# Performance work log

Measured on AMD Instinct MI355X. Metric: run time of the kernel, lower is better.

Reference implementation:

```python
import jax, jax.numpy as jnp
import numpy as np

HIDDEN = 1024
VOCAB = 50257


def setup_inputs() -> dict:
    key = jax.random.key(0)
    ks = jax.random.split(key, 9)
    s = 0.02
    return {
        "token": jax.random.randint(ks[0], (1,), 0, VOCAB, dtype=jnp.int64),
        "hidden": jax.random.normal(ks[1], (1, 1, HIDDEN), dtype=jnp.float32),
        "emb": jax.random.normal(ks[2], (VOCAB, HIDDEN), dtype=jnp.float32) * s,
        "w_ih": jax.random.normal(ks[3], (3 * HIDDEN, HIDDEN), dtype=jnp.float32) * s,
        "w_hh": jax.random.normal(ks[4], (3 * HIDDEN, HIDDEN), dtype=jnp.float32) * s,
        "b_ih": jax.random.normal(ks[5], (3 * HIDDEN,), dtype=jnp.float32) * s,
        "b_hh": jax.random.normal(ks[6], (3 * HIDDEN,), dtype=jnp.float32) * s,
        "w_out": jax.random.normal(ks[7], (VOCAB, HIDDEN), dtype=jnp.float32) * s,
        "b_out": jax.random.normal(ks[8], (VOCAB,), dtype=jnp.float32) * s,
    }


def reference(token, hidden, emb, w_ih, w_hh, b_ih, b_hh, w_out, b_out):
    # embed + relu: [1, H]
    x = jax.nn.relu(emb[token].reshape(1, HIDDEN))
    h = hidden[0]  # [1, H]
    # single-step GRU (PyTorch gate order r, z, n; separate biases)
    gi = x @ w_ih.T + b_ih  # [1, 3H]
    gh = h @ w_hh.T + b_hh  # [1, 3H]
    i_r, i_z, i_n = jnp.split(gi, 3, axis=-1)
    h_r, h_z, h_n = jnp.split(gh, 3, axis=-1)
    r = jax.nn.sigmoid(i_r + h_r)
    z = jax.nn.sigmoid(i_z + h_z)
    n = jnp.tanh(i_n + r * h_n)
    h_new = (1.0 - z) * n + z * h  # [1, H]
    # output projection + log-softmax over vocab
    logits = h_new @ w_out.T + b_out  # [1, V]
    logp = jax.nn.log_softmax(logits, axis=1)
    return logp, h_new[None]  # ([1, V], [1, 1, H])
```

## Files before the change

kernel.cpp:

```cpp
#include <hip/hip_runtime.h>
#include <math.h>

#define HIDDEN 1024
#define VOCAB 50257
#define K2_BLOCKS 2048
#define NW (K2_BLOCKS * 4)

typedef float f32x4 __attribute__((ext_vector_type(4)));

__device__ __forceinline__ float wave_reduce_sum(float v) {
#pragma unroll
    for (int m = 1; m < 64; m <<= 1) v += __shfl_xor(v, m, 64);
    return v;
}

__device__ __forceinline__ float dot4(f32x4 a, f32x4 b) {
    return a.x * b.x + a.y * b.y + a.z * b.z + a.w * b.w;
}

__global__ __launch_bounds__(192) void gru_kernel(
    const int* token_p, const float* __restrict__ hidden, const float* __restrict__ emb,
    const float* __restrict__ w_ih, const float* __restrict__ w_hh,
    const float* __restrict__ b_ih, const float* __restrict__ b_hh,
    float* __restrict__ h_new_out, float* __restrict__ h_new_ws) {
    const int g = threadIdx.x >> 6;
    const int lane = threadIdx.x & 63;
    const int j = blockIdx.x;

    const int token = token_p[0];
    const f32x4* x4 = (const f32x4*)(emb + (size_t)token * HIDDEN);
    const f32x4* h4 = (const f32x4*)hidden;
    const f32x4* wi = (const f32x4*)(w_ih + (size_t)(g * HIDDEN + j) * HIDDEN);
    const f32x4* wh = (const f32x4*)(w_hh + (size_t)(g * HIDDEN + j) * HIDDEN);

    float acc_i = 0.f, acc_h = 0.f;
#pragma unroll
    for (int k = 0; k < 4; ++k) {
        const int idx = k * 64 + lane;
        f32x4 e = x4[idx];
        f32x4 h = h4[idx];
        f32x4 a = __builtin_nontemporal_load(wi + idx);
        f32x4 b = __builtin_nontemporal_load(wh + idx);
        e.x = fmaxf(e.x, 0.f); e.y = fmaxf(e.y, 0.f);
        e.z = fmaxf(e.z, 0.f); e.w = fmaxf(e.w, 0.f);
        acc_i += dot4(a, e);
        acc_h += dot4(b, h);
    }
    acc_i = wave_reduce_sum(acc_i);
    acc_h = wave_reduce_sum(acc_h);

    __shared__ float red_i[3], red_h[3];
    if (lane == 0) { red_i[g] = acc_i; red_h[g] = acc_h; }
    __syncthreads();

    if (threadIdx.x == 0) {
        const float i_r = red_i[0] + b_ih[j];
        const float i_z = red_i[1] + b_ih[HIDDEN + j];
        const float i_n = red_i[2] + b_ih[2 * HIDDEN + j];
        const float h_r = red_h[0] + b_hh[j];
        const float h_z = red_h[1] + b_hh[HIDDEN + j];
        const float h_n = red_h[2] + b_hh[2 * HIDDEN + j];
        const float r = 1.f / (1.f + expf(-(i_r + h_r)));
        const float z = 1.f / (1.f + expf(-(i_z + h_z)));
        const float n = tanhf(i_n + r * h_n);
        const float hv = (1.f - z) * n + z * hidden[j];
        h_new_out[j] = hv;
        h_new_ws[j] = hv;
    }
}

__global__ __launch_bounds__(256) void logits_kernel(
    const float* __restrict__ h_new, const float* __restrict__ w_out,
    const float* __restrict__ b_out, float* __restrict__ logits,
    float* __restrict__ partials) {
    const int wave = threadIdx.x >> 6;
    const int lane = threadIdx.x & 63;
    const int gw = blockIdx.x * 4 + wave;

    const int BASE = VOCAB / NW;
    const int EXTRA = VOCAB - BASE * NW;
    const int start = gw * BASE + (gw < EXTRA ? gw : EXTRA);
    const int end = start + BASE + (gw < EXTRA ? 1 : 0);

    const f32x4* h4 = (const f32x4*)h_new;
    f32x4 hs[4];
#pragma unroll
    for (int k = 0; k < 4; ++k) hs[k] = h4[k * 64 + lane];

    float m = -INFINITY, s = 0.f;
    int v = start;

    for (; v + 3 < end; v += 4) {
        const f32x4* w0 = (const f32x4*)(w_out + (size_t)v * HIDDEN);
        float a0 = 0.f, a1 = 0.f, a2 = 0.f, a3 = 0.f;
#pragma unroll
        for (int k = 0; k < 4; ++k) {
            const int idx = k * 64 + lane;
            f32x4 x0 = __builtin_nontemporal_load(w0 + idx);
            f32x4 x1 = __builtin_nontemporal_load(w0 + 256 + idx);
            f32x4 x2 = __builtin_nontemporal_load(w0 + 512 + idx);
            f32x4 x3 = __builtin_nontemporal_load(w0 + 768 + idx);
            a0 += dot4(x0, hs[k]);
            a1 += dot4(x1, hs[k]);
            a2 += dot4(x2, hs[k]);
            a3 += dot4(x3, hs[k]);
        }
        a0 = wave_reduce_sum(a0);
        a1 = wave_reduce_sum(a1);
        a2 = wave_reduce_sum(a2);
        a3 = wave_reduce_sum(a3);
        const float l0 = a0 + b_out[v];
        const float l1 = a1 + b_out[v + 1];
        const float l2 = a2 + b_out[v + 2];
        const float l3 = a3 + b_out[v + 3];
        if (lane == 0) {
            logits[v] = l0; logits[v + 1] = l1;
            logits[v + 2] = l2; logits[v + 3] = l3;
        }
        const float mx = fmaxf(fmaxf(l0, l1), fmaxf(l2, l3));
        if (mx > m) { s *= expf(m - mx); m = mx; }
        s += expf(l0 - m) + expf(l1 - m) + expf(l2 - m) + expf(l3 - m);
    }
    for (; v + 1 < end; v += 2) {
        const f32x4* w0 = (const f32x4*)(w_out + (size_t)v * HIDDEN);
        float a0 = 0.f, a1 = 0.f;
#pragma unroll
        for (int k = 0; k < 4; ++k) {
            const int idx = k * 64 + lane;
            f32x4 x0 = __builtin_nontemporal_load(w0 + idx);
            f32x4 x1 = __builtin_nontemporal_load(w0 + 256 + idx);
            a0 += dot4(x0, hs[k]);
            a1 += dot4(x1, hs[k]);
        }
        a0 = wave_reduce_sum(a0);
        a1 = wave_reduce_sum(a1);
        const float l0 = a0 + b_out[v];
        const float l1 = a1 + b_out[v + 1];
        if (lane == 0) { logits[v] = l0; logits[v + 1] = l1; }
        const float mx = fmaxf(l0, l1);
        if (mx > m) { s *= expf(m - mx); m = mx; }
        s += expf(l0 - m) + expf(l1 - m);
    }
    if (v < end) {
        const f32x4* w0 = (const f32x4*)(w_out + (size_t)v * HIDDEN);
        float a0 = 0.f;
#pragma unroll
        for (int k = 0; k < 4; ++k) {
            f32x4 x0 = __builtin_nontemporal_load(w0 + k * 64 + lane);
            a0 += dot4(x0, hs[k]);
        }
        a0 = wave_reduce_sum(a0);
        const float l0 = a0 + b_out[v];
        if (lane == 0) logits[v] = l0;
        if (l0 > m) { s *= expf(m - l0); m = l0; }
        s += expf(l0 - m);
    }

    __shared__ float sm[4], ss[4];
    if (lane == 0) { sm[wave] = m; ss[wave] = s; }
    __syncthreads();
    if (threadIdx.x == 0) {
        float M = fmaxf(fmaxf(sm[0], sm[1]), fmaxf(sm[2], sm[3]));
        float S = ss[0] * expf(sm[0] - M) + ss[1] * expf(sm[1] - M) +
                  ss[2] * expf(sm[2] - M) + ss[3] * expf(sm[3] - M);
        partials[2 * blockIdx.x] = M;
        partials[2 * blockIdx.x + 1] = S;
    }
}

__global__ __launch_bounds__(256) void finalize_kernel(
    const float* __restrict__ partials, float* __restrict__ logits) {
    const int t = threadIdx.x;
    const int wave = t >> 6;
    const int lane = t & 63;

    float m = -INFINITY, s = 0.f;
#pragma unroll
    for (int i = 0; i < K2_BLOCKS / 256; ++i) {
        const int idx = i * 256 + t;
        const float pm = partials[2 * idx];
        const float ps = partials[2 * idx + 1];
        const float M = fmaxf(m, pm);
        s = s * expf(m - M) + ps * expf(pm - M);
        m = M;
    }
#pragma unroll
    for (int o = 1; o < 64; o <<= 1) {
        const float pm = __shfl_xor(m, o, 64);
        const float ps = __shfl_xor(s, o, 64);
        const float M = fmaxf(m, pm);
        s = s * expf(m - M) + ps * expf(pm - M);
        m = M;
    }
    __shared__ float sm[4], ss[4];
    if (lane == 0) { sm[wave] = m; ss[wave] = s; }
    __syncthreads();
    const float M = fmaxf(fmaxf(sm[0], sm[1]), fmaxf(sm[2], sm[3]));
    const float S = ss[0] * expf(sm[0] - M) + ss[1] * expf(sm[1] - M) +
                    ss[2] * expf(sm[2] - M) + ss[3] * expf(sm[3] - M);
    const float c = M + logf(S);

    float4* l4 = (float4*)logits;
    const int n4 = VOCAB / 4;
    for (int i = blockIdx.x * 256 + t; i < n4; i += gridDim.x * 256) {
        float4 x = l4[i];
        x.x -= c; x.y -= c; x.z -= c; x.w -= c;
        l4[i] = x;
    }
    if (blockIdx.x == 0 && t == 0) logits[VOCAB - 1] -= c;
}

extern "C" void kernel_launch(void* const* d_in, const int* in_sizes, int n_in,
                              void* d_out, int out_size, void* d_ws, size_t ws_size,
                              hipStream_t stream) {
    const int*   token  = (const int*)d_in[0];
    const float* hidden = (const float*)d_in[1];
    const float* emb    = (const float*)d_in[2];
    const float* w_ih   = (const float*)d_in[3];
    const float* w_hh   = (const float*)d_in[4];
    const float* b_ih   = (const float*)d_in[5];
    const float* b_hh   = (const float*)d_in[6];
    const float* w_out  = (const float*)d_in[7];
    const float* b_out  = (const float*)d_in[8];

    float* out      = (float*)d_out;
    float* h_new    = out + VOCAB;
    float* logits   = out;
    float* ws       = (float*)d_ws;
    float* partials = ws;
    float* h_new_ws = ws + 2 * K2_BLOCKS;

    gru_kernel<<<HIDDEN, 192, 0, stream>>>(token, hidden, emb, w_ih, w_hh,
                                           b_ih, b_hh, h_new, h_new_ws);
    logits_kernel<<<K2_BLOCKS, 256, 0, stream>>>(h_new_ws, w_out, b_out, logits,
                                                 partials);
    finalize_kernel<<<64, 256, 0, stream>>>(partials, logits);
}
```

Baseline: 44.79 us.

## Split GRU dot products across six waves and use fast exp intrinsics

The GRU kernel now uses 384 threads so each wave handles one gate row for either the input or the hidden stream, instead of one wave doing both. The 4-row unrolled path in the logits kernel is removed, leaving 2-row iterations. All expf calls become __expf, and tanh is computed from exp. The finalize grid doubles to 128 blocks. Less unrolling may reduce memory-level parallelism in the dominant w_out stream, and the fast exp slightly changes accuracy.

```diff
diff --git a/kernel.cpp b/kernel.cpp
--- a/kernel.cpp
+++ b/kernel.cpp
@@ -18,51 +18,53 @@
     return a.x * b.x + a.y * b.y + a.z * b.z + a.w * b.w;
 }
 
-__global__ __launch_bounds__(192) void gru_kernel(
+__global__ __launch_bounds__(384) void gru_kernel(
     const int* token_p, const float* __restrict__ hidden, const float* __restrict__ emb,
     const float* __restrict__ w_ih, const float* __restrict__ w_hh,
     const float* __restrict__ b_ih, const float* __restrict__ b_hh,
     float* __restrict__ h_new_out, float* __restrict__ h_new_ws) {
-    const int g = threadIdx.x >> 6;
+    const int w = threadIdx.x >> 6;
+    const int g = (w < 3) ? w : (w - 3);
+    const int hstream = (w >= 3);
     const int lane = threadIdx.x & 63;
     const int j = blockIdx.x;
 
     const int token = token_p[0];
-    const f32x4* x4 = (const f32x4*)(emb + (size_t)token * HIDDEN);
-    const f32x4* h4 = (const f32x4*)hidden;
-    const f32x4* wi = (const f32x4*)(w_ih + (size_t)(g * HIDDEN + j) * HIDDEN);
-    const f32x4* wh = (const f32x4*)(w_hh + (size_t)(g * HIDDEN + j) * HIDDEN);
-
-    float acc_i = 0.f, acc_h = 0.f;
+    const f32x4* vec = hstream ? (const f32x4*)hidden
+                               : (const f32x4*)(emb + (size_t)token * HIDDEN);
+    const f32x4* wrow = hstream
+        ? (const f32x4*)(w_hh + (size_t)(g * HIDDEN + j) * HIDDEN)
+        : (const f32x4*)(w_ih + (size_t)(g * HIDDEN + j) * HIDDEN);
+
+    float acc = 0.f;
 #pragma unroll
     for (int k = 0; k < 4; ++k) {
         const int idx = k * 64 + lane;
-        f32x4 e = x4[idx];
-        f32x4 h = h4[idx];
-        f32x4 a = __builtin_nontemporal_load(wi + idx);
-        f32x4 b = __builtin_nontemporal_load(wh + idx);
-        e.x = fmaxf(e.x, 0.f); e.y = fmaxf(e.y, 0.f);
-        e.z = fmaxf(e.z, 0.f); e.w = fmaxf(e.w, 0.f);
-        acc_i += dot4(a, e);
-        acc_h += dot4(b, h);
-    }
-    acc_i = wave_reduce_sum(acc_i);
-    acc_h = wave_reduce_sum(acc_h);
-
-    __shared__ float red_i[3], red_h[3];
-    if (lane == 0) { red_i[g] = acc_i; red_h[g] = acc_h; }
+        f32x4 x = vec[idx];
+        f32x4 a = __builtin_nontemporal_load(wrow + idx);
+        if (!hstream) {
+            x.x = fmaxf(x.x, 0.f); x.y = fmaxf(x.y, 0.f);
+            x.z = fmaxf(x.z, 0.f); x.w = fmaxf(x.w, 0.f);
+        }
+        acc += dot4(a, x);
+    }
+    acc = wave_reduce_sum(acc);
+
+    __shared__ float red[6];
+    if (lane == 0) red[w] = acc;
     __syncthreads();
 
     if (threadIdx.x == 0) {
-        const float i_r = red_i[0] + b_ih[j];
-        const float i_z = red_i[1] + b_ih[HIDDEN + j];
-        const float i_n = red_i[2] + b_ih[2 * HIDDEN + j];
-        const float h_r = red_h[0] + b_hh[j];
-        const float h_z = red_h[1] + b_hh[HIDDEN + j];
-        const float h_n = red_h[2] + b_hh[2 * HIDDEN + j];
-        const float r = 1.f / (1.f + expf(-(i_r + h_r)));
-        const float z = 1.f / (1.f + expf(-(i_z + h_z)));
-        const float n = tanhf(i_n + r * h_n);
+        const float i_r = red[0] + b_ih[j];
+        const float i_z = red[1] + b_ih[HIDDEN + j];
+        const float i_n = red[2] + b_ih[2 * HIDDEN + j];
+        const float h_r = red[3] + b_hh[j];
+        const float h_z = red[4] + b_hh[HIDDEN + j];
+        const float h_n = red[5] + b_hh[2 * HIDDEN + j];
+        const float r = 1.f / (1.f + __expf(-(i_r + h_r)));
+        const float z = 1.f / (1.f + __expf(-(i_z + h_z)));
+        const float targ = i_n + r * h_n;
+        const float n = 1.f - 2.f / (__expf(2.f * targ) + 1.f);
         const float hv = (1.f - z) * n + z * hidden[j];
         h_new_out[j] = hv;
         h_new_ws[j] = hv;
@@ -89,38 +91,6 @@
 
     float m = -INFINITY, s = 0.f;
     int v = start;
-
-    for (; v + 3 < end; v += 4) {
-        const f32x4* w0 = (const f32x4*)(w_out + (size_t)v * HIDDEN);
-        float a0 = 0.f, a1 = 0.f, a2 = 0.f, a3 = 0.f;
-#pragma unroll
-        for (int k = 0; k < 4; ++k) {
-            const int idx = k * 64 + lane;
-            f32x4 x0 = __builtin_nontemporal_load(w0 + idx);
-            f32x4 x1 = __builtin_nontemporal_load(w0 + 256 + idx);
-            f32x4 x2 = __builtin_nontemporal_load(w0 + 512 + idx);
-            f32x4 x3 = __builtin_nontemporal_load(w0 + 768 + idx);
-            a0 += dot4(x0, hs[k]);
-            a1 += dot4(x1, hs[k]);
-            a2 += dot4(x2, hs[k]);
-            a3 += dot4(x3, hs[k]);
-        }
-        a0 = wave_reduce_sum(a0);
-        a1 = wave_reduce_sum(a1);
-        a2 = wave_reduce_sum(a2);
-        a3 = wave_reduce_sum(a3);
-        const float l0 = a0 + b_out[v];
-        const float l1 = a1 + b_out[v + 1];
-        const float l2 = a2 + b_out[v + 2];
-        const float l3 = a3 + b_out[v + 3];
-        if (lane == 0) {
-            logits[v] = l0; logits[v + 1] = l1;
-            logits[v + 2] = l2; logits[v + 3] = l3;
-        }
-        const float mx = fmaxf(fmaxf(l0, l1), fmaxf(l2, l3));
-        if (mx > m) { s *= expf(m - mx); m = mx; }
-        s += expf(l0 - m) + expf(l1 - m) + expf(l2 - m) + expf(l3 - m);
-    }
     for (; v + 1 < end; v += 2) {
         const f32x4* w0 = (const f32x4*)(w_out + (size_t)v * HIDDEN);
         float a0 = 0.f, a1 = 0.f;
@@ -138,8 +108,8 @@
         const float l1 = a1 + b_out[v + 1];
         if (lane == 0) { logits[v] = l0; logits[v + 1] = l1; }
         const float mx = fmaxf(l0, l1);
-        if (mx > m) { s *= expf(m - mx); m = mx; }
-        s += expf(l0 - m) + expf(l1 - m);
+        if (mx > m) { s *= __expf(m - mx); m = mx; }
+        s += __expf(l0 - m) + __expf(l1 - m);
     }
     if (v < end) {
         const f32x4* w0 = (const f32x4*)(w_out + (size_t)v * HIDDEN);
@@ -152,8 +122,8 @@
         a0 = wave_reduce_sum(a0);
         const float l0 = a0 + b_out[v];
         if (lane == 0) logits[v] = l0;
-        if (l0 > m) { s *= expf(m - l0); m = l0; }
-        s += expf(l0 - m);
+        if (l0 > m) { s *= __expf(m - l0); m = l0; }
+        s += __expf(l0 - m);
     }
 
     __shared__ float sm[4], ss[4];
@@ -161,8 +131,8 @@
     __syncthreads();
     if (threadIdx.x == 0) {
         float M = fmaxf(fmaxf(sm[0], sm[1]), fmaxf(sm[2], sm[3]));
-        float S = ss[0] * expf(sm[0] - M) + ss[1] * expf(sm[1] - M) +
-                  ss[2] * expf(sm[2] - M) + ss[3] * expf(sm[3] - M);
+        float S = ss[0] * __expf(sm[0] - M) + ss[1] * __expf(sm[1] - M) +
+                  ss[2] * __expf(sm[2] - M) + ss[3] * __expf(sm[3] - M);
         partials[2 * blockIdx.x] = M;
         partials[2 * blockIdx.x + 1] = S;
     }
@@ -181,7 +151,7 @@
         const float pm = partials[2 * idx];
         const float ps = partials[2 * idx + 1];
         const float M = fmaxf(m, pm);
-        s = s * expf(m - M) + ps * expf(pm - M);
+        s = s * __expf(m - M) + ps * __expf(pm - M);
         m = M;
     }
 #pragma unroll
@@ -189,15 +159,15 @@
         const float pm = __shfl_xor(m, o, 64);
         const float ps = __shfl_xor(s, o, 64);
         const float M = fmaxf(m, pm);
-        s = s * expf(m - M) + ps * expf(pm - M);
+        s = s * __expf(m - M) + ps * __expf(pm - M);
         m = M;
     }
     __shared__ float sm[4], ss[4];
     if (lane == 0) { sm[wave] = m; ss[wave] = s; }
     __syncthreads();
     const float M = fmaxf(fmaxf(sm[0], sm[1]), fmaxf(sm[2], sm[3]));
-    const float S = ss[0] * expf(sm[0] - M) + ss[1] * expf(sm[1] - M) +
-                    ss[2] * expf(sm[2] - M) + ss[3] * expf(sm[3] - M);
+    const float S = ss[0] * __expf(sm[0] - M) + ss[1] * __expf(sm[1] - M) +
+                    ss[2] * __expf(sm[2] - M) + ss[3] * __expf(sm[3] - M);
     const float c = M + logf(S);
 
     float4* l4 = (float4*)logits;
@@ -230,9 +200,9 @@
     float* partials = ws;
     float* h_new_ws = ws + 2 * K2_BLOCKS;
 
-    gru_kernel<<<HIDDEN, 192, 0, stream>>>(token, hidden, emb, w_ih, w_hh,
+    gru_kernel<<<HIDDEN, 384, 0, stream>>>(token, hidden, emb, w_ih, w_hh,
                                            b_ih, b_hh, h_new, h_new_ws);
     logits_kernel<<<K2_BLOCKS, 256, 0, stream>>>(h_new_ws, w_out, b_out, logits,
                                                  partials);
-    finalize_kernel<<<64, 256, 0, stream>>>(partials, logits);
-}
+    finalize_kernel<<<128, 256, 0, stream>>>(partials, logits);
+}
```

New measurement: 45.75 us. 1.02x slower.
